# Optimization experiments

Hardware: AMD Instinct MI355X
Metric: run time of the kernel (lower is better)

## Reference

```python
import jax, jax.numpy as jnp
import numpy as np

# constants from VMD_block.__init__ (K=4, alpha=2000, tau=0, DC=0, init=1, tol=5e-5, max_N=5)
K = 4
ALPHA = 2000.0
TAU = 0.0
TOL = 5e-05
MAX_N = 5


def _mvmd(f):
    """Multivariate VMD (Rehman & Aftab 2019) on f: (C, T) real signals.
    Returns modes u: (K, C, T). Shared center frequencies omega across channels."""
    C, T = f.shape
    half = T // 2
    T2 = 2 * T
    # mirror extension to length 2T
    fM = jnp.concatenate([f[:, :half][:, ::-1], f, f[:, half:][:, ::-1]], axis=1)
    freqs = (jnp.arange(1, T2 + 1, dtype=f.dtype) / T2) - 0.5 - (1.0 / T2)  # (T2,)
    f_hat = jnp.fft.fftshift(jnp.fft.fft(fM, axis=1), axes=1).astype(jnp.complex64)
    h2 = T2 // 2
    f_hat_plus = f_hat.at[:, :h2].set(0.0)  # keep analytic (positive-freq) part
    fpos = freqs[h2:]

    omega0 = (0.5 / K) * jnp.arange(K, dtype=f.dtype)  # init == 1, DC == 0
    u0 = jnp.zeros((K, C, T2), dtype=jnp.complex64)
    lam0 = jnp.zeros((C, T2), dtype=jnp.complex64)

    def cond(st):
        _, _, _, n, uDiff = st
        return jnp.logical_and(uDiff > TOL, n < MAX_N)

    def body(st):
        u, omega, lam, n, _ = st
        u_prev = u
        sum_all = jnp.sum(u, axis=0)  # (C, T2)
        for k in range(K):  # Gauss-Seidel mode updates; K is small & static
            sum_uk = sum_all - u[k]
            denom = 1.0 + ALPHA * (freqs - omega[k]) ** 2  # (T2,)
            u_k = (f_hat_plus - sum_uk - lam / 2.0) / denom
            sum_all = sum_uk + u_k
            u = u.at[k].set(u_k)
            power = jnp.abs(u_k[:, h2:]) ** 2  # (C, T2/2) positive freqs
            omega = omega.at[k].set(jnp.sum(fpos * power) / jnp.sum(power))
        lam = lam + TAU * (sum_all - f_hat_plus)  # tau == 0 -> dual ascent is a no-op
        d = u - u_prev
        uDiff = jnp.abs(jnp.sum(d * jnp.conj(d)) / T2) + jnp.finfo(jnp.float32).eps
        return u, omega, lam, n + 1, uDiff.astype(jnp.float32)

    st0 = (u0, omega0, lam0, jnp.int32(0), jnp.float32(TOL + 1.0))
    u, omega, lam, n, uDiff = jax.lax.while_loop(cond, body, st0)

    # rebuild full spectrum via Hermitian symmetry, back to time domain
    u_hat = jnp.zeros((K, C, T2), dtype=jnp.complex64)
    u_hat = u_hat.at[:, :, h2:].set(u[:, :, h2:])
    u_hat = u_hat.at[:, :, 1:h2 + 1].set(jnp.conj(u[:, :, h2:])[:, :, ::-1])
    u_hat = u_hat.at[:, :, 0].set(jnp.conj(u_hat[:, :, -1]))
    ut = jnp.real(jnp.fft.ifft(jnp.fft.ifftshift(u_hat, axes=-1), axis=-1))
    return ut[:, :, T2 // 4: 3 * T2 // 4]  # crop mirror padding -> (K, C, T)


def setup_inputs() -> dict:
    key = jax.random.key(0)
    x = jax.random.normal(key, (8, 2048, 64), dtype=jnp.float32)  # (B, T, C)
    return {"x": x}


def reference(x):
    B, T, C = x.shape
    xr = jnp.transpose(x, (0, 2, 1)).reshape(B * C, T)  # (B*C, T)
    u = _mvmd(xr)  # (K, B*C, T)
    x_l = jnp.transpose(u[0].reshape(B, C, T), (0, 2, 1))  # lowest-freq mode -> (B, T, C)
    x_h = x - x_l
    return (x_h, x_l)
```

## Files before the change

### kernel.cpp

```cpp
#include <hip/hip_runtime.h>
#include <math.h>

#define TLEN 2048
#define T2   4096
#define H2   2048
#define NBLK 512
#define EPS32 1.1920928955078125e-07

__device__ __forceinline__ double ld_acc(const double* p){
  return __hip_atomic_load(p, __ATOMIC_RELAXED, __HIP_MEMORY_SCOPE_AGENT);
}
__device__ __forceinline__ unsigned ld_u32(const unsigned* p){
  return __hip_atomic_load(p, __ATOMIC_RELAXED, __HIP_MEMORY_SCOPE_AGENT);
}
__device__ __forceinline__ void st_u32(unsigned* p, unsigned v){
  __hip_atomic_store(p, v, __ATOMIC_RELAXED, __HIP_MEMORY_SCOPE_AGENT);
}

__device__ void tree_sync_omega(unsigned* leaf, unsigned* root, unsigned* rec,
                                const double* slot, float* somf, int gid){
  unsigned old = __hip_atomic_fetch_add(leaf + (size_t)gid * 32, 1u,
                                        __ATOMIC_RELAXED, __HIP_MEMORY_SCOPE_AGENT);
  if (old == 63u){
    unsigned oldr = __hip_atomic_fetch_add(root, 1u,
                                           __ATOMIC_RELAXED, __HIP_MEMORY_SCOPE_AGENT);
    if (oldr == 7u){
      double uD = ld_acc(slot + 8);
      float o0 = (float)(ld_acc(slot + 0) / ld_acc(slot + 4));
      float o1 = (float)(ld_acc(slot + 1) / ld_acc(slot + 5));
      float o2 = (float)(ld_acc(slot + 2) / ld_acc(slot + 6));
      float o3 = (float)(ld_acc(slot + 3) / ld_acc(slot + 7));
      unsigned fl = (uD * (1.0 / 4096.0) + EPS32 > 5e-5) ? 3u : 1u;
      st_u32(rec + 1, __float_as_uint(o0));
      st_u32(rec + 2, __float_as_uint(o1));
      st_u32(rec + 3, __float_as_uint(o2));
      st_u32(rec + 4, __float_as_uint(o3));
      __hip_atomic_store(rec, fl, __ATOMIC_RELEASE, __HIP_MEMORY_SCOPE_AGENT);
    }
  }
  unsigned f, spins = 0;
  while (((f = ld_u32(rec)) & 1u) == 0u){
    if (++spins > (1u << 22)) break;
    __builtin_amdgcn_s_sleep(2);
  }
  somf[7] = (f & 2u) ? 1.f : 0.f;
  somf[0] = __uint_as_float(ld_u32(rec + 1));
  somf[1] = __uint_as_float(ld_u32(rec + 2));
  somf[2] = __uint_as_float(ld_u32(rec + 3));
  somf[3] = __uint_as_float(ld_u32(rec + 4));
}

#define R2REG(ZA, ZB, W, SGN, E, O) {                           \
  float wy_ = (SGN) * W.y;                                      \
  E = make_float2(ZA.x + ZB.x, ZA.y + ZB.y);                    \
  float dx_ = ZA.x - ZB.x, dy_ = ZA.y - ZB.y;                   \
  O = make_float2(dx_ * W.x - dy_ * wy_, dx_ * wy_ + dy_ * W.x); }

#define R4REG(A, B, C, D, W1, W2, W3, SGN, Y0, Y1, Y2, Y3) {    \
  float w1y_ = (SGN)*W1.y, w2y_ = (SGN)*W2.y, w3y_ = (SGN)*W3.y;\
  float t0x = A.x + C.x, t0y = A.y + C.y;                       \
  float t1x = A.x - C.x, t1y = A.y - C.y;                       \
  float t2x = B.x + D.x, t2y = B.y + D.y;                       \
  float t3x = (SGN) * (B.y - D.y), t3y = -(SGN) * (B.x - D.x);  \
  Y0 = make_float2(t0x + t2x, t0y + t2y);                       \
  float y1x = t1x + t3x, y1y = t1y + t3y;                       \
  float y2x = t0x - t2x, y2y = t0y - t2y;                       \
  float y3x = t1x - t3x, y3y = t1y - t3y;                       \
  Y1 = make_float2(y1x*W1.x - y1y*w1y_, y1x*w1y_ + y1y*W1.x);   \
  Y2 = make_float2(y2x*W2.x - y2y*w2y_, y2x*w2y_ + y2y*W2.x);   \
  Y3 = make_float2(y3x*W3.x - y3y*w3y_, y3x*w3y_ + y3y*W3.x); }

__device__ __forceinline__ void fused2(float2 z0, float2 z1, float2 z2, float2 z3,
                                       float2 z4, float2 z5, float2 z6, float2 z7,
                                       const float2* twl, float sgn, float2* dst){
  const int tid = threadIdx.x;
  float2 wa = twl[2*tid], wb = twl[2*tid+512], wc = twl[2*tid+1024], wd = twl[2*tid+1536];
  float2 e0,o0,e1,o1,e2,o2,e3,o3;
  R2REG(z0, z4, wa, sgn, e0, o0)
  R2REG(z1, z5, wb, sgn, e1, o1)
  R2REG(z2, z6, wc, sgn, e2, o2)
  R2REG(z3, z7, wd, sgn, e3, o3)
  float2 w1 = twl[4*tid], w2 = twl[8*tid], w3 = twl[12*tid];
  float2 a0,a1,a2,a3, b0,b1,b2,b3;
  R4REG(e0, e1, e2, e3, w1, w2, w3, sgn, a0, a1, a2, a3)
  R4REG(o0, o1, o2, o3, w1, w2, w3, sgn, b0, b1, b2, b3)
  float4* d4 = reinterpret_cast<float4*>(dst + 8 * tid);
  d4[0] = make_float4(a0.x, a0.y, b0.x, b0.y);
  d4[1] = make_float4(a1.x, a1.y, b1.x, b1.y);
  d4[2] = make_float4(a2.x, a2.y, b2.x, b2.y);
  d4[3] = make_float4(a3.x, a3.y, b3.x, b3.y);
}

__device__ __forceinline__ void r4_stages(float2* src, float2* dst,
                                          const float2* twl, float sgn,
                                          int first, int cnt){
  const int tid = threadIdx.x;
  #pragma unroll 1
  for (int t = 0; t < cnt; ++t){
    const int L = 2 << (2 * (first + t));
    const int Lm = L - 1;
    #pragma unroll
    for (int bf = 0; bf < 2; ++bf){
      int idx = tid + (bf << 8);
      int q  = idx & Lm;
      int tb = idx - q;
      float2 a = src[idx];
      float2 b = src[idx + 512];
      float2 c = src[idx + 1024];
      float2 d = src[idx + 1536];
      float2 w1 = twl[2 * tb];
      float2 w2 = twl[4 * tb];
      float2 w3 = twl[6 * tb];
      float2 y0, y1, y2, y3;
      R4REG(a, b, c, d, w1, w2, w3, sgn, y0, y1, y2, y3)
      int ob = q + (tb << 2);
      dst[ob]         = y0;
      dst[ob + L]     = y1;
      dst[ob + 2 * L] = y2;
      dst[ob + 3 * L] = y3;
    }
    __syncthreads();
    float2* tt = src; src = dst; dst = tt;
  }
}

__device__ __forceinline__ float wredf(float v){
  #pragma unroll
  for (int off = 32; off; off >>= 1) v += __shfl_down(v, off);
  return v;
}

__device__ __forceinline__ void red9(float a0, float a1, float a2, float a3,
                                     float a4, float a5, float a6, float a7,
                                     float a8, float* redf, double* accs){
  const int tid = threadIdx.x, wave = tid >> 6, lane = tid & 63;
  float r;
  r = wredf(a0); if (lane == 0) redf[ 0 + wave] = r;
  r = wredf(a1); if (lane == 0) redf[ 4 + wave] = r;
  r = wredf(a2); if (lane == 0) redf[ 8 + wave] = r;
  r = wredf(a3); if (lane == 0) redf[12 + wave] = r;
  r = wredf(a4); if (lane == 0) redf[16 + wave] = r;
  r = wredf(a5); if (lane == 0) redf[20 + wave] = r;
  r = wredf(a6); if (lane == 0) redf[24 + wave] = r;
  r = wredf(a7); if (lane == 0) redf[28 + wave] = r;
  r = wredf(a8); if (lane == 0) redf[32 + wave] = r;
  __syncthreads();
  if (tid < 9){
    double s = (double)redf[tid*4+0] + (double)redf[tid*4+1]
             + (double)redf[tid*4+2] + (double)redf[tid*4+3];
    atomicAdd(&accs[tid], s);
  }
}

#define MODE_S(UXc, UYc, OMc, AFP, AP) {                       \
  float ox_ = sx - (UXc), oy_ = sy - (UYc);                    \
  float d_  = fj - (OMc);                                      \
  float rden_ = __builtin_amdgcn_rcpf(fmaf(2000.0f * d_, d_, 1.0f)); \
  float nx_ = (Fx - ox_) * rden_, ny_ = (Fy - oy_) * rden_;    \
  float pw_ = nx_ * nx_ + ny_ * ny_;                           \
  AFP += fj * pw_;  AP += pw_;                                 \
  float ddx_ = nx_ - (UXc), ddy_ = ny_ - (UYc);                \
  aD += ddx_ * ddx_ + ddy_ * ddy_;                             \
  (UXc) = nx_; (UYc) = ny_;                                    \
  sx = ox_ + nx_; sy = oy_ + ny_; }

#define BIN_S(PP, FV, UX, UY) {                                \
  float Fx = FV.x, Fy = FV.y;                                  \
  float fj = (float)(tid + ((PP) << 8)) * (1.0f / 4096.0f);    \
  float sx = UX.x + UX.y + UX.z + UX.w;                        \
  float sy = UY.x + UY.y + UY.z + UY.w;                        \
  MODE_S(UX.x, UY.x, om.x, aFP0, aP0)                          \
  MODE_S(UX.y, UY.y, om.y, aFP1, aP1)                          \
  MODE_S(UX.z, UY.z, om.z, aFP2, aP2)                          \
  MODE_S(UX.w, UY.w, om.w, aFP3, aP3) }

#define IT1(PP, FV, UX, UY) { UX = make_float4(0.f,0.f,0.f,0.f); \
                              UY = make_float4(0.f,0.f,0.f,0.f); \
                              BIN_S(PP, FV, UX, UY) }

#define FCOMP(PP, FV) {                                        \
  int k = tid + ((PP) << 8);                                   \
  float2 A  = bufA[k];                                         \
  float2 Zm = bufA[(2048 - k) & 2047];                         \
  float px = 0.5f * (A.x + Zm.x), py = 0.5f * (A.y - Zm.y);    \
  float qx = 0.5f * (A.x - Zm.x), qy = 0.5f * (A.y + Zm.y);    \
  float2 W = twl[k];                                           \
  FV = make_float2(px + W.x * qy + W.y * qx,                   \
                   py - W.x * qx + W.y * qy); }

#define HERMU(PP, FV, UX, UY) {                                \
  int j = tid + ((PP) << 8);                                   \
  float vx, vy;                                                \
  if (act){                                                    \
    float sx = UX.y + UX.z + UX.w;                             \
    float sy = UY.y + UY.z + UY.w;                             \
    float fj = (float)j * (1.0f / 4096.0f);                    \
    float dd = fj - om0;                                       \
    float rden = __builtin_amdgcn_rcpf(fmaf(2000.0f * dd, dd, 1.0f)); \
    vx = (FV.x - sx) * rden; vy = (FV.y - sy) * rden;          \
  } else { vx = UX.x; vy = UY.x; }                             \
  bufA[j] = make_float2(vx, vy); }

#define ZPCOMP(PP, ZV) {                                       \
  int k = tid + ((PP) << 8);                                   \
  if (k == 0){                                                 \
    float e = bufA[0].x + bufA[2047].x;                        \
    float o = bufA[0].x - bufA[2047].x;                        \
    ZV = make_float2(e, o);                                    \
  } else {                                                     \
    float2 A  = bufA[k];                                       \
    float2 Bm = bufA[2048 - k];                                \
    float ex = A.x + Bm.x, ey = A.y - Bm.y;                    \
    float dx = A.x - Bm.x, dy = A.y + Bm.y;                    \
    float2 W = twl[k];                                         \
    float ox = dx * W.x + dy * W.y;                            \
    float oy = dy * W.x - dx * W.y;                            \
    ZV = make_float2(ex - oy, ey + ox);                        \
  } }

#define FOR8F(M) M(0,f0,ux0,uy0) M(1,f1,ux1,uy1) M(2,f2,ux2,uy2) M(3,f3,ux3,uy3) \
                 M(4,f4,ux4,uy4) M(5,f5,ux5,uy5) M(6,f6,ux6,uy6) M(7,f7,ux7,uy7)

#define ILAST(IDX, Y1, Y2) {                                   \
  float2 a = bufA[IDX];                                        \
  float2 bb = bufA[(IDX) + 512];                               \
  float2 c = bufA[(IDX) + 1024];                               \
  float2 d = bufA[(IDX) + 1536];                               \
  float t1x = a.x - c.x, t1y = a.y - c.y;                      \
  float t3x = -(bb.y - d.y), t3y = (bb.x - d.x);               \
  Y1 = make_float2(t1x + t3x, t1y + t3y);                      \
  float t0x = a.x + c.x, t0y = a.y + c.y;                      \
  float t2x = bb.x + d.x, t2y = bb.y + d.y;                    \
  Y2 = make_float2(t0x - t2x, t0y - t2y); }

__global__ void __attribute__((amdgpu_flat_work_group_size(256, 256),
                               amdgpu_waves_per_eu(2, 2)))
k_main(const float* __restrict__ x, unsigned* __restrict__ leaf,
       unsigned* __restrict__ root, unsigned* __restrict__ rec,
       double* __restrict__ accs, float* __restrict__ xh, float* __restrict__ xl){
  __shared__ float2 twl[3072];
  __shared__ float2 bufA[H2];
  __shared__ float2 bufB[H2];
  __shared__ float redf[36];
  __shared__ float somf[8];
  const int tid = threadIdx.x;
  const int b = blockIdx.x & 7, ch = blockIdx.x >> 3;
  const int gid = blockIdx.x & 7;
  const float* xc = x + (size_t)b * TLEN * 64 + ch;

  #pragma unroll
  for (int i = 0; i < 12; ++i){
    int p = tid + (i << 8);
    float rev = (float)p * (-1.0f / 4096.0f);
    twl[p] = make_float2(__builtin_amdgcn_cosf(rev), __builtin_amdgcn_sinf(rev));
  }

  float2 z0, z1, z2, z3, z4, z5, z6, z7;
  z0 = make_float2(xc[(size_t)(1023 - 2*tid) * 64], xc[(size_t)(1022 - 2*tid) * 64]);
  z1 = make_float2(xc[(size_t)( 511 - 2*tid) * 64], xc[(size_t)( 510 - 2*tid) * 64]);
  { int t = 2*tid;        z2 = make_float2(xc[(size_t)t*64], xc[(size_t)(t+1)*64]); }
  { int t = 2*tid + 512;  z3 = make_float2(xc[(size_t)t*64], xc[(size_t)(t+1)*64]); }
  { int t = 2*tid + 1024; z4 = make_float2(xc[(size_t)t*64], xc[(size_t)(t+1)*64]); }
  { int t = 2*tid + 1536; z5 = make_float2(xc[(size_t)t*64], xc[(size_t)(t+1)*64]); }
  z6 = make_float2(xc[(size_t)(2047 - 2*tid) * 64], xc[(size_t)(2046 - 2*tid) * 64]);
  z7 = make_float2(xc[(size_t)(1535 - 2*tid) * 64], xc[(size_t)(1534 - 2*tid) * 64]);
  __syncthreads();

  fused2(z0, z1, z2, z3, z4, z5, z6, z7, twl, 1.0f, bufA);
  __syncthreads();
  r4_stages(bufA, bufB, twl, 1.0f, 1, 4);

  float2 f0, f1, f2, f3, f4, f5, f6, f7;
  FCOMP(0, f0) FCOMP(1, f1) FCOMP(2, f2) FCOMP(3, f3)
  FCOMP(4, f4) FCOMP(5, f5) FCOMP(6, f6) FCOMP(7, f7)

  float4 ux0, ux1, ux2, ux3, ux4, ux5, ux6, ux7;
  float4 uy0, uy1, uy2, uy3, uy4, uy5, uy6, uy7;
  float4 om = make_float4(0.0f, 0.125f, 0.25f, 0.375f);

  {
    float aFP0=0,aFP1=0,aFP2=0,aFP3=0,aP0=0,aP1=0,aP2=0,aP3=0,aD=0;
    FOR8F(IT1)
    red9(aFP0,aFP1,aFP2,aFP3,aP0,aP1,aP2,aP3,aD, redf, accs);
  }

  bool active = true;
  #pragma unroll 1
  for (int it = 0; it < 3; ++it){
    __syncthreads();
    if (tid == 0)
      tree_sync_omega(leaf + it * 256, root + it * 32, rec + it * 32,
                      accs + it * 16, somf, gid);
    __syncthreads();
    if (active){
      if (somf[7] != 0.0f){
        om.x = somf[0]; om.y = somf[1]; om.z = somf[2]; om.w = somf[3];
      } else active = false;
    }
    if (active){
      float aFP0=0,aFP1=0,aFP2=0,aFP3=0,aP0=0,aP1=0,aP2=0,aP3=0,aD=0;
      FOR8F(BIN_S)
      red9(aFP0,aFP1,aFP2,aFP3,aP0,aP1,aP2,aP3,aD, redf, accs + (it + 1) * 16);
    }
  }
  __syncthreads();
  if (tid == 0)
    tree_sync_omega(leaf + 3 * 256, root + 3 * 32, rec + 3 * 32,
                    accs + 3 * 16, somf, gid);
  __syncthreads();

  {
    bool act = active && (somf[7] != 0.0f);
    float om0 = somf[0];
    FOR8F(HERMU)
    __syncthreads();
    float2 p0, p1, p2, p3, p4, p5, p6, p7;
    ZPCOMP(0, p0) ZPCOMP(1, p1) ZPCOMP(2, p2) ZPCOMP(3, p3)
    ZPCOMP(4, p4) ZPCOMP(5, p5) ZPCOMP(6, p6) ZPCOMP(7, p7)
    __syncthreads();
    fused2(p0, p1, p2, p3, p4, p5, p6, p7, twl, -1.0f, bufB);
    __syncthreads();
    r4_stages(bufB, bufA, twl, -1.0f, 1, 3);
  }

  {
    const float scale = 1.0f / 4096.0f;
    float2 y1a, y2a, y1b, y2b;
    ILAST(tid,       y1a, y2a)
    ILAST(tid + 256, y1b, y2b)
    #define STOUT(YV, T0, ZS) {                                \
      size_t o0 = ((size_t)(b * TLEN + (T0))) * 64 + ch;       \
      float l0 = YV.x * scale, l1 = YV.y * scale;              \
      xh[o0]      = ZS.x - l0;  xl[o0]      = l0;              \
      xh[o0 + 64] = ZS.y - l1;  xl[o0 + 64] = l1; }
    STOUT(y1a, 2*tid,        z2)
    STOUT(y1b, 2*tid + 512,  z3)
    STOUT(y2a, 2*tid + 1024, z4)
    STOUT(y2b, 2*tid + 1536, z5)
  }
}

extern "C" void kernel_launch(void* const* d_in, const int* in_sizes, int n_in,
                              void* d_out, int out_size, void* d_ws, size_t ws_size,
                              hipStream_t stream){
  const float* x = (const float*)d_in[0];
  float* out_xh = (float*)d_out;
  float* out_xl = out_xh + (size_t)8 * TLEN * 64;

  char* ws = (char*)d_ws;
  unsigned* leaf = (unsigned*)ws;
  unsigned* root = (unsigned*)(ws + 4096);
  unsigned* rec  = (unsigned*)(ws + 4608);
  double*   accs = (double*)  (ws + 5120);

  hipMemsetAsync(ws, 0, 5632, stream);
  k_main<<<NBLK, 256, 0, stream>>>(x, leaf, root, rec, accs, out_xh, out_xl);
}
```

Baseline: 123.5 us.

## Exploit mirror symmetry to run VMD on real cosine-transform coefficients

```diff
diff --git a/kernel.cpp b/kernel.cpp
--- a/kernel.cpp
+++ b/kernel.cpp
@@ -1,9 +1,6 @@
 #include <hip/hip_runtime.h>
 #include <math.h>
 
-#define TLEN 2048
-#define T2   4096
-#define H2   2048
 #define NBLK 512
 #define EPS32 1.1920928955078125e-07
 
@@ -50,12 +47,6 @@
   somf[3] = __uint_as_float(ld_u32(rec + 4));
 }
 
-#define R2REG(ZA, ZB, W, SGN, E, O) {                           \
-  float wy_ = (SGN) * W.y;                                      \
-  E = make_float2(ZA.x + ZB.x, ZA.y + ZB.y);                    \
-  float dx_ = ZA.x - ZB.x, dy_ = ZA.y - ZB.y;                   \
-  O = make_float2(dx_ * W.x - dy_ * wy_, dx_ * wy_ + dy_ * W.x); }
-
 #define R4REG(A, B, C, D, W1, W2, W3, SGN, Y0, Y1, Y2, Y3) {    \
   float w1y_ = (SGN)*W1.y, w2y_ = (SGN)*W2.y, w3y_ = (SGN)*W3.y;\
   float t0x = A.x + C.x, t0y = A.y + C.y;                       \
@@ -70,55 +61,29 @@
   Y2 = make_float2(y2x*W2.x - y2y*w2y_, y2x*w2y_ + y2y*W2.x);   \
   Y3 = make_float2(y3x*W3.x - y3y*w3y_, y3x*w3y_ + y3y*W3.x); }
 
-__device__ __forceinline__ void fused2(float2 z0, float2 z1, float2 z2, float2 z3,
-                                       float2 z4, float2 z5, float2 z6, float2 z7,
-                                       const float2* twl, float sgn, float2* dst){
-  const int tid = threadIdx.x;
-  float2 wa = twl[2*tid], wb = twl[2*tid+512], wc = twl[2*tid+1024], wd = twl[2*tid+1536];
-  float2 e0,o0,e1,o1,e2,o2,e3,o3;
-  R2REG(z0, z4, wa, sgn, e0, o0)
-  R2REG(z1, z5, wb, sgn, e1, o1)
-  R2REG(z2, z6, wc, sgn, e2, o2)
-  R2REG(z3, z7, wd, sgn, e3, o3)
-  float2 w1 = twl[4*tid], w2 = twl[8*tid], w3 = twl[12*tid];
-  float2 a0,a1,a2,a3, b0,b1,b2,b3;
-  R4REG(e0, e1, e2, e3, w1, w2, w3, sgn, a0, a1, a2, a3)
-  R4REG(o0, o1, o2, o3, w1, w2, w3, sgn, b0, b1, b2, b3)
-  float4* d4 = reinterpret_cast<float4*>(dst + 8 * tid);
-  d4[0] = make_float4(a0.x, a0.y, b0.x, b0.y);
-  d4[1] = make_float4(a1.x, a1.y, b1.x, b1.y);
-  d4[2] = make_float4(a2.x, a2.y, b2.x, b2.y);
-  d4[3] = make_float4(a3.x, a3.y, b3.x, b3.y);
-}
-
-__device__ __forceinline__ void r4_stages(float2* src, float2* dst,
-                                          const float2* twl, float sgn,
-                                          int first, int cnt){
+__device__ __forceinline__ void r4s(float2* src, float2* dst,
+                                    const float2* twl, float sgn, int cnt){
   const int tid = threadIdx.x;
   #pragma unroll 1
   for (int t = 0; t < cnt; ++t){
-    const int L = 2 << (2 * (first + t));
+    const int L = 4 << (2 * t);
     const int Lm = L - 1;
-    #pragma unroll
-    for (int bf = 0; bf < 2; ++bf){
-      int idx = tid + (bf << 8);
-      int q  = idx & Lm;
-      int tb = idx - q;
-      float2 a = src[idx];
-      float2 b = src[idx + 512];
-      float2 c = src[idx + 1024];
-      float2 d = src[idx + 1536];
-      float2 w1 = twl[2 * tb];
-      float2 w2 = twl[4 * tb];
-      float2 w3 = twl[6 * tb];
-      float2 y0, y1, y2, y3;
-      R4REG(a, b, c, d, w1, w2, w3, sgn, y0, y1, y2, y3)
-      int ob = q + (tb << 2);
-      dst[ob]         = y0;
-      dst[ob + L]     = y1;
-      dst[ob + 2 * L] = y2;
-      dst[ob + 3 * L] = y3;
-    }
+    int q  = tid & Lm;
+    int tb = tid - q;
+    float2 a = src[tid];
+    float2 b = src[tid + 256];
+    float2 c = src[tid + 512];
+    float2 d = src[tid + 768];
+    float2 w1 = twl[tb];
+    float2 w2 = twl[2 * tb];
+    float2 w3 = twl[3 * tb];
+    float2 y0, y1, y2, y3;
+    R4REG(a, b, c, d, w1, w2, w3, sgn, y0, y1, y2, y3)
+    int ob = q + (tb << 2);
+    dst[ob]         = y0;
+    dst[ob + L]     = y1;
+    dst[ob + 2 * L] = y2;
+    dst[ob + 3 * L] = y3;
     __syncthreads();
     float2* tt = src; src = dst; dst = tt;
   }
@@ -152,135 +117,111 @@
   }
 }
 
-#define MODE_S(UXc, UYc, OMc, AFP, AP) {                       \
-  float ox_ = sx - (UXc), oy_ = sy - (UYc);                    \
-  float d_  = fj - (OMc);                                      \
-  float rden_ = __builtin_amdgcn_rcpf(fmaf(2000.0f * d_, d_, 1.0f)); \
-  float nx_ = (Fx - ox_) * rden_, ny_ = (Fy - oy_) * rden_;    \
-  float pw_ = nx_ * nx_ + ny_ * ny_;                           \
+#define MODE_R(RC, OMC, AFP, AP) {                             \
+  float o_ = s - (RC);                                         \
+  float d_ = fj - (OMC);                                       \
+  float rd_ = __builtin_amdgcn_rcpf(fmaf(2000.0f*d_, d_, 1.0f));\
+  float n_ = (RR - o_) * rd_;                                  \
+  float pw_ = n_ * n_;                                         \
   AFP += fj * pw_;  AP += pw_;                                 \
-  float ddx_ = nx_ - (UXc), ddy_ = ny_ - (UYc);                \
-  aD += ddx_ * ddx_ + ddy_ * ddy_;                             \
-  (UXc) = nx_; (UYc) = ny_;                                    \
-  sx = ox_ + nx_; sy = oy_ + ny_; }
-
-#define BIN_S(PP, FV, UX, UY) {                                \
-  float Fx = FV.x, Fy = FV.y;                                  \
-  float fj = (float)(tid + ((PP) << 8)) * (1.0f / 4096.0f);    \
-  float sx = UX.x + UX.y + UX.z + UX.w;                        \
-  float sy = UY.x + UY.y + UY.z + UY.w;                        \
-  MODE_S(UX.x, UY.x, om.x, aFP0, aP0)                          \
-  MODE_S(UX.y, UY.y, om.y, aFP1, aP1)                          \
-  MODE_S(UX.z, UY.z, om.z, aFP2, aP2)                          \
-  MODE_S(UX.w, UY.w, om.w, aFP3, aP3) }
-
-#define IT1(PP, FV, UX, UY) { UX = make_float4(0.f,0.f,0.f,0.f); \
-                              UY = make_float4(0.f,0.f,0.f,0.f); \
-                              BIN_S(PP, FV, UX, UY) }
-
-#define FCOMP(PP, FV) {                                        \
-  int k = tid + ((PP) << 8);                                   \
-  float2 A  = bufA[k];                                         \
-  float2 Zm = bufA[(2048 - k) & 2047];                         \
-  float px = 0.5f * (A.x + Zm.x), py = 0.5f * (A.y - Zm.y);    \
-  float qx = 0.5f * (A.x - Zm.x), qy = 0.5f * (A.y + Zm.y);    \
-  float2 W = twl[k];                                           \
-  FV = make_float2(px + W.x * qy + W.y * qx,                   \
-                   py - W.x * qx + W.y * qy); }
-
-#define HERMU(PP, FV, UX, UY) {                                \
-  int j = tid + ((PP) << 8);                                   \
-  float vx, vy;                                                \
+  float dd_ = n_ - (RC);  aD += dd_ * dd_;                     \
+  (RC) = n_;  s = o_ + n_; }
+
+#define RBIN(RHO, RRv, FJ) {                                   \
+  float RR = RRv;  float fj = FJ;                              \
+  float s = RHO.x + RHO.y + RHO.z + RHO.w;                     \
+  MODE_R(RHO.x, om.x, aFP0, aP0)                               \
+  MODE_R(RHO.y, om.y, aFP1, aP1)                               \
+  MODE_R(RHO.z, om.z, aFP2, aP2)                               \
+  MODE_R(RHO.w, om.w, aFP3, aP3) }
+
+#define IT1R(RHO, RRv, FJ) { RHO = make_float4(0.f,0.f,0.f,0.f); RBIN(RHO, RRv, FJ) }
+
+#define FOR8R(M) M(r0,R0,fj0) M(r1,R1,fj1) M(r2,R2,fj2) M(r3,R3,fj3) \
+                 M(r4,R4,fj4) M(r5,R5,fj5) M(r6,R6,fj6) M(r7,R7,fj7)
+
+#define C5(RHO, RRv, FJ, CV) {                                 \
   if (act){                                                    \
-    float sx = UX.y + UX.z + UX.w;                             \
-    float sy = UY.y + UY.z + UY.w;                             \
-    float fj = (float)j * (1.0f / 4096.0f);                    \
-    float dd = fj - om0;                                       \
-    float rden = __builtin_amdgcn_rcpf(fmaf(2000.0f * dd, dd, 1.0f)); \
-    vx = (FV.x - sx) * rden; vy = (FV.y - sy) * rden;          \
-  } else { vx = UX.x; vy = UY.x; }                             \
-  bufA[j] = make_float2(vx, vy); }
-
-#define ZPCOMP(PP, ZV) {                                       \
-  int k = tid + ((PP) << 8);                                   \
-  if (k == 0){                                                 \
-    float e = bufA[0].x + bufA[2047].x;                        \
-    float o = bufA[0].x - bufA[2047].x;                        \
-    ZV = make_float2(e, o);                                    \
-  } else {                                                     \
-    float2 A  = bufA[k];                                       \
-    float2 Bm = bufA[2048 - k];                                \
-    float ex = A.x + Bm.x, ey = A.y - Bm.y;                    \
-    float dx = A.x - Bm.x, dy = A.y + Bm.y;                    \
-    float2 W = twl[k];                                         \
-    float ox = dx * W.x + dy * W.y;                            \
-    float oy = dy * W.x - dx * W.y;                            \
-    ZV = make_float2(ex - oy, ey + ox);                        \
-  } }
-
-#define FOR8F(M) M(0,f0,ux0,uy0) M(1,f1,ux1,uy1) M(2,f2,ux2,uy2) M(3,f3,ux3,uy3) \
-                 M(4,f4,ux4,uy4) M(5,f5,ux5,uy5) M(6,f6,ux6,uy6) M(7,f7,ux7,uy7)
-
-#define ILAST(IDX, Y1, Y2) {                                   \
-  float2 a = bufA[IDX];                                        \
-  float2 bb = bufA[(IDX) + 512];                               \
-  float2 c = bufA[(IDX) + 1024];                               \
-  float2 d = bufA[(IDX) + 1536];                               \
-  float t1x = a.x - c.x, t1y = a.y - c.y;                      \
-  float t3x = -(bb.y - d.y), t3y = (bb.x - d.x);               \
-  Y1 = make_float2(t1x + t3x, t1y + t3y);                      \
-  float t0x = a.x + c.x, t0y = a.y + c.y;                      \
-  float t2x = bb.x + d.x, t2y = bb.y + d.y;                    \
-  Y2 = make_float2(t0x - t2x, t0y - t2y); }
+    float o_ = RHO.y + RHO.z + RHO.w;                          \
+    float d_ = FJ - om0;                                       \
+    float rd_ = __builtin_amdgcn_rcpf(fmaf(2000.0f*d_, d_, 1.0f));\
+    CV = (RRv - o_) * rd_;                                     \
+  } else CV = RHO.x; }
 
 __global__ void __attribute__((amdgpu_flat_work_group_size(256, 256),
                                amdgpu_waves_per_eu(2, 2)))
 k_main(const float* __restrict__ x, unsigned* __restrict__ leaf,
        unsigned* __restrict__ root, unsigned* __restrict__ rec,
        double* __restrict__ accs, float* __restrict__ xh, float* __restrict__ xl){
-  __shared__ float2 twl[3072];
-  __shared__ float2 bufA[H2];
-  __shared__ float2 bufB[H2];
+  __shared__ float2 twl[768];
+  __shared__ float2 bufA[1024];
+  __shared__ float2 bufB[1024];
   __shared__ float redf[36];
   __shared__ float somf[8];
+  __shared__ float2 vNy;
+  __shared__ float sKs;
   const int tid = threadIdx.x;
   const int b = blockIdx.x & 7, ch = blockIdx.x >> 3;
   const int gid = blockIdx.x & 7;
-  const float* xc = x + (size_t)b * TLEN * 64 + ch;
+  const float* xc = x + (size_t)b * 2048 * 64 + ch;
 
   #pragma unroll
-  for (int i = 0; i < 12; ++i){
+  for (int i = 0; i < 3; ++i){
     int p = tid + (i << 8);
-    float rev = (float)p * (-1.0f / 4096.0f);
+    float rev = (float)p * (-1.0f / 1024.0f);
     twl[p] = make_float2(__builtin_amdgcn_cosf(rev), __builtin_amdgcn_sinf(rev));
   }
 
-  float2 z0, z1, z2, z3, z4, z5, z6, z7;
-  z0 = make_float2(xc[(size_t)(1023 - 2*tid) * 64], xc[(size_t)(1022 - 2*tid) * 64]);
-  z1 = make_float2(xc[(size_t)( 511 - 2*tid) * 64], xc[(size_t)( 510 - 2*tid) * 64]);
-  { int t = 2*tid;        z2 = make_float2(xc[(size_t)t*64], xc[(size_t)(t+1)*64]); }
-  { int t = 2*tid + 512;  z3 = make_float2(xc[(size_t)t*64], xc[(size_t)(t+1)*64]); }
-  { int t = 2*tid + 1024; z4 = make_float2(xc[(size_t)t*64], xc[(size_t)(t+1)*64]); }
-  { int t = 2*tid + 1536; z5 = make_float2(xc[(size_t)t*64], xc[(size_t)(t+1)*64]); }
-  z6 = make_float2(xc[(size_t)(2047 - 2*tid) * 64], xc[(size_t)(2046 - 2*tid) * 64]);
-  z7 = make_float2(xc[(size_t)(1535 - 2*tid) * 64], xc[(size_t)(1534 - 2*tid) * 64]);
-  __syncthreads();
-
-  fused2(z0, z1, z2, z3, z4, z5, z6, z7, twl, 1.0f, bufA);
-  __syncthreads();
-  r4_stages(bufA, bufB, twl, 1.0f, 1, 4);
-
-  float2 f0, f1, f2, f3, f4, f5, f6, f7;
-  FCOMP(0, f0) FCOMP(1, f1) FCOMP(2, f2) FCOMP(3, f3)
-  FCOMP(4, f4) FCOMP(5, f5) FCOMP(6, f6) FCOMP(7, f7)
-
-  float4 ux0, ux1, ux2, ux3, ux4, ux5, ux6, ux7;
-  float4 uy0, uy1, uy2, uy3, uy4, uy5, uy6, uy7;
+  float2 za = make_float2(xc[(size_t)(4*tid       ) * 64], xc[(size_t)(4*tid + 2   ) * 64]);
+  float2 zb = make_float2(xc[(size_t)(4*tid + 1024) * 64], xc[(size_t)(4*tid + 1026) * 64]);
+  float2 zc = make_float2(xc[(size_t)(2047 - 4*tid) * 64], xc[(size_t)(2045 - 4*tid) * 64]);
+  float2 zd = make_float2(xc[(size_t)(1023 - 4*tid) * 64], xc[(size_t)(1021 - 4*tid) * 64]);
+  __syncthreads();
+
+  {
+    float2 w1 = twl[tid], w2 = twl[2*tid], w3 = twl[3*tid];
+    float2 y0, y1, y2, y3;
+    R4REG(za, zb, zc, zd, w1, w2, w3, 1.0f, y0, y1, y2, y3)
+    float4* d4 = reinterpret_cast<float4*>(bufA + 4 * tid);
+    d4[0] = make_float4(y0.x, y0.y, y1.x, y1.y);
+    d4[1] = make_float4(y2.x, y2.y, y3.x, y3.y);
+  }
+  __syncthreads();
+  r4s(bufA, bufB, twl, 1.0f, 4);
+
+  float R0,R1,R2,R3,R4,R5,R6,R7, fj0,fj1,fj2,fj3,fj4,fj5,fj6,fj7;
+  #define UNPK(C, RA, RB, FA, FB) {                            \
+    int k = tid + ((C) << 8);                                  \
+    float2 Zk = bufA[k];                                       \
+    float2 Zm = bufA[(1024 - k) & 1023];                       \
+    float px = 0.5f*(Zk.x + Zm.x), py = 0.5f*(Zk.y - Zm.y);    \
+    float qx = 0.5f*(Zk.x - Zm.x), qy = 0.5f*(Zk.y + Zm.y);    \
+    float rw = (float)k * (-1.0f / 2048.0f);                   \
+    float Wx = __builtin_amdgcn_cosf(rw), Wy = __builtin_amdgcn_sinf(rw); \
+    float Vx = px + Wx*qy + Wy*qx;                             \
+    float Vy = py - Wx*qx + Wy*qy;                             \
+    float re = (float)k * (-1.0f / 8192.0f);                   \
+    float Ex = __builtin_amdgcn_cosf(re), Ey = __builtin_amdgcn_sinf(re); \
+    RA = 2.0f * (Ex*Vx - Ey*Vy);                               \
+    RB = -2.0f * (Ex*Vy + Ey*Vx);                              \
+    FA = (float)k * (1.0f/4096.0f);                            \
+    FB = (float)(2048 - k) * (1.0f/4096.0f); }
+  UNPK(0, R0, R1, fj0, fj1)
+  UNPK(1, R2, R3, fj2, fj3)
+  UNPK(2, R4, R5, fj4, fj5)
+  UNPK(3, R6, R7, fj6, fj7)
+  if (tid == 0){
+    float2 Z0 = bufA[0];
+    R1 = 1.41421356237f * (Z0.x - Z0.y);
+    fj1 = 0.25f;
+  }
+
+  float4 r0, r1, r2, r3, r4, r5, r6, r7;
   float4 om = make_float4(0.0f, 0.125f, 0.25f, 0.375f);
 
   {
     float aFP0=0,aFP1=0,aFP2=0,aFP3=0,aP0=0,aP1=0,aP2=0,aP3=0,aD=0;
-    FOR8F(IT1)
+    FOR8R(IT1R)
     red9(aFP0,aFP1,aFP2,aFP3,aP0,aP1,aP2,aP3,aD, redf, accs);
   }
 
@@ -299,7 +240,7 @@
     }
     if (active){
       float aFP0=0,aFP1=0,aFP2=0,aFP3=0,aP0=0,aP1=0,aP2=0,aP3=0,aD=0;
-      FOR8F(BIN_S)
+      FOR8R(RBIN)
       red9(aFP0,aFP1,aFP2,aFP3,aP0,aP1,aP2,aP3,aD, redf, accs + (it + 1) * 16);
     }
   }
@@ -312,31 +253,71 @@
   {
     bool act = active && (somf[7] != 0.0f);
     float om0 = somf[0];
-    FOR8F(HERMU)
-    __syncthreads();
-    float2 p0, p1, p2, p3, p4, p5, p6, p7;
-    ZPCOMP(0, p0) ZPCOMP(1, p1) ZPCOMP(2, p2) ZPCOMP(3, p3)
-    ZPCOMP(4, p4) ZPCOMP(5, p5) ZPCOMP(6, p6) ZPCOMP(7, p7)
-    __syncthreads();
-    fused2(p0, p1, p2, p3, p4, p5, p6, p7, twl, -1.0f, bufB);
-    __syncthreads();
-    r4_stages(bufB, bufA, twl, -1.0f, 1, 3);
-  }
-
-  {
-    const float scale = 1.0f / 4096.0f;
-    float2 y1a, y2a, y1b, y2b;
-    ILAST(tid,       y1a, y2a)
-    ILAST(tid + 256, y1b, y2b)
-    #define STOUT(YV, T0, ZS) {                                \
-      size_t o0 = ((size_t)(b * TLEN + (T0))) * 64 + ch;       \
-      float l0 = YV.x * scale, l1 = YV.y * scale;              \
-      xh[o0]      = ZS.x - l0;  xl[o0]      = l0;              \
-      xh[o0 + 64] = ZS.y - l1;  xl[o0 + 64] = l1; }
-    STOUT(y1a, 2*tid,        z2)
-    STOUT(y1b, 2*tid + 512,  z3)
-    STOUT(y2a, 2*tid + 1024, z4)
-    STOUT(y2b, 2*tid + 1536, z5)
+    float c0, c1, c2, c3, c4, c5, c6, c7;
+    C5(r0, R0, fj0, c0)  C5(r1, R1, fj1, c1)
+    C5(r2, R2, fj2, c2)  C5(r3, R3, fj3, c3)
+    C5(r4, R4, fj4, c4)  C5(r5, R5, fj5, c5)
+    C5(r6, R6, fj6, c6)  C5(r7, R7, fj7, c7)
+    if (tid == 1) sKs = c1;
+    if (tid == 0) vNy = make_float2(1.41421356237f * c1, 0.0f);
+    #define VPW(C, CA, CB) {                                   \
+      int k = tid + ((C) << 8);                                \
+      float rg = (float)k * (1.0f / 8192.0f);                  \
+      float Gx = __builtin_amdgcn_cosf(rg), Gy = __builtin_amdgcn_sinf(rg); \
+      bufA[k] = make_float2(Gx*(CA) + Gy*(CB), Gy*(CA) - Gx*(CB)); }
+    VPW(0, c0, c1)  VPW(1, c2, c3)  VPW(2, c4, c5)  VPW(3, c6, c7)
+    if (tid == 0) bufA[0] = make_float2(c0, 0.0f);
+  }
+  __syncthreads();
+  float2 p0, p1, p2, p3;
+  #define ZB(C, ZV) {                                          \
+    int q = tid + ((C) << 8);                                  \
+    float2 Vq = bufA[q];                                       \
+    float2 Vm = (q == 0) ? vNy : bufA[1024 - q];               \
+    Vm.y = -Vm.y;                                              \
+    float Ex_ = Vq.x + Vm.x, Ey_ = Vq.y + Vm.y;                \
+    float Dx = Vq.x - Vm.x,  Dy = Vq.y - Vm.y;                 \
+    float rw = (float)q * (1.0f / 2048.0f);                    \
+    float Wx = __builtin_amdgcn_cosf(rw), Wy = __builtin_amdgcn_sinf(rw); \
+    float Ox = Dx*Wx - Dy*Wy;                                  \
+    float Oy = Dx*Wy + Dy*Wx;                                  \
+    ZV = make_float2(Ex_ - Oy, Ey_ + Ox); }
+  ZB(0, p0)  ZB(1, p1)  ZB(2, p2)  ZB(3, p3)
+  {
+    float2 w1 = twl[tid], w2 = twl[2*tid], w3 = twl[3*tid];
+    float2 y0, y1, y2, y3;
+    R4REG(p0, p1, p2, p3, w1, w2, w3, -1.0f, y0, y1, y2, y3)
+    float4* d4 = reinterpret_cast<float4*>(bufB + 4 * tid);
+    d4[0] = make_float4(y0.x, y0.y, y1.x, y1.y);
+    d4[1] = make_float4(y2.x, y2.y, y3.x, y3.y);
+  }
+  __syncthreads();
+  r4s(bufB, bufA, twl, -1.0f, 3);
+
+  {
+    float2 a = bufA[tid], bb = bufA[tid + 256];
+    float2 c = bufA[tid + 512], d = bufA[tid + 768];
+    float t0x = a.x + c.x, t0y = a.y + c.y;
+    float t1x = a.x - c.x, t1y = a.y - c.y;
+    float t2x = bb.x + d.x, t2y = bb.y + d.y;
+    float t3x = -(bb.y - d.y), t3y = (bb.x - d.x);
+    float2 y0 = make_float2(t0x + t2x, t0y + t2y);
+    float2 y1 = make_float2(t1x + t3x, t1y + t3y);
+    float2 y2 = make_float2(t0x - t2x, t0y - t2y);
+    float2 y3 = make_float2(t1x - t3x, t1y - t3y);
+    const float sc = 1.0f / 4096.0f;
+    float kc = sKs * (0.99999970586f * sc);
+    #define OUT2(YV, T0, T1, KS, ZS) {                         \
+      size_t oa = ((size_t)(b * 2048 + (T0))) * 64 + ch;       \
+      size_t ob = ((size_t)(b * 2048 + (T1))) * 64 + ch;       \
+      float l0 = YV.x * sc KS kc;                              \
+      float l1 = YV.y * sc KS kc;                              \
+      xl[oa] = l0;  xh[oa] = ZS.x - l0;                        \
+      xl[ob] = l1;  xh[ob] = ZS.y - l1; }
+    OUT2(y0, 4*tid,        4*tid + 2,    -, za)
+    OUT2(y1, 4*tid + 1024, 4*tid + 1026, -, zb)
+    OUT2(y2, 2047 - 4*tid, 2045 - 4*tid, +, zc)
+    OUT2(y3, 1023 - 4*tid, 1021 - 4*tid, +, zd)
   }
 }
 
@@ -345,7 +326,7 @@
                               hipStream_t stream){
   const float* x = (const float*)d_in[0];
   float* out_xh = (float*)d_out;
-  float* out_xl = out_xh + (size_t)8 * TLEN * 64;
+  float* out_xl = out_xh + (size_t)8 * 2048 * 64;
 
   char* ws = (char*)d_ws;
   unsigned* leaf = (unsigned*)ws;
```

New measurement: 118.7 us. 1.04x faster.
